# Kernel optimization log

Measured on AMD Instinct MI355X. Metric: run time of the kernel, lower is better.

The kernel has to match this reference:

```python
import jax, jax.numpy as jnp
import numpy as np

N_NODES = 50000
N_EDGES = 800000
IN_C = 16
HID_C = 16
OUT_C = 10
N_GRAPHS = 500
EDGE_DIM = 3
MLP_HID = 25
BN_EPS = 1e-5


def setup_inputs() -> dict:
    key = jax.random.key(0)
    ks = iter(jax.random.split(key, 40))

    def nrm(shape, scale=1.0):
        return jax.random.normal(next(ks), shape, dtype=jnp.float32) * scale

    inp = {}
    inp["x"] = nrm((N_NODES, IN_C))
    inp["edge_index"] = jax.random.randint(next(ks), (2, N_EDGES), 0, N_NODES, dtype=jnp.int32)
    inp["edge_attr"] = jax.random.uniform(next(ks), (N_EDGES, EDGE_DIM), dtype=jnp.float32)
    inp["batch"] = jnp.sort(jax.random.randint(next(ks), (N_NODES,), 0, N_GRAPHS, dtype=jnp.int32))

    def bn_params():
        g = jax.random.uniform(next(ks), (MLP_HID,), minval=0.8, maxval=1.2, dtype=jnp.float32)
        b = nrm((MLP_HID,), 0.1)
        mu = nrm((MLP_HID,), 0.1)
        var = jax.random.uniform(next(ks), (MLP_HID,), minval=0.5, maxval=1.5, dtype=jnp.float32)
        return g, b, mu, var

    # edge MLP 1: 3 -> 25 -> IN_C*HID_C
    inp["W1a"] = nrm((EDGE_DIM, MLP_HID), 0.3)
    inp["b1a"] = nrm((MLP_HID,), 0.05)
    inp["g1"], inp["bt1"], inp["m1"], inp["v1"] = bn_params()
    inp["W1b"] = nrm((MLP_HID, IN_C * HID_C), 0.1)
    inp["b1b"] = nrm((IN_C * HID_C,), 0.05)
    inp["root1"] = nrm((IN_C, HID_C), 0.2)
    inp["bias1"] = nrm((HID_C,), 0.05)

    # edge MLP 2: 3 -> 25 -> HID_C*HID_C
    inp["W2a"] = nrm((EDGE_DIM, MLP_HID), 0.3)
    inp["b2a"] = nrm((MLP_HID,), 0.05)
    inp["g2"], inp["bt2"], inp["m2"], inp["v2"] = bn_params()
    inp["W2b"] = nrm((MLP_HID, HID_C * HID_C), 0.1)
    inp["b2b"] = nrm((HID_C * HID_C,), 0.05)
    inp["root2"] = nrm((HID_C, HID_C), 0.2)
    inp["bias2"] = nrm((HID_C,), 0.05)

    # final MLP([HID_C, OUT_C]) -> single plain linear (plain_last)
    inp["fcW"] = nrm((HID_C, OUT_C), 0.2)
    inp["fcb"] = nrm((OUT_C,), 0.05)
    return inp


def _edge_mlp(e, Wa, ba, g, bt, mu, var, Wb, bb):
    # Linear -> BatchNorm(eval) -> ReLU -> (dropout=eval identity) -> Linear
    h = e @ Wa + ba
    h = g * (h - mu) * jax.lax.rsqrt(var + BN_EPS) + bt
    h = jax.nn.relu(h)
    return h @ Wb + bb


def _nnconv(x, src, dst, w_edge, root, bias, out_dim):
    # message: x_j [E,in] times per-edge weight [E,in,out]
    msg = jnp.einsum("ei,eio->eo", x[src], w_edge)
    agg = jax.ops.segment_sum(msg, dst, num_segments=N_NODES)
    deg = jax.ops.segment_sum(jnp.ones((src.shape[0],), msg.dtype), dst, num_segments=N_NODES)
    agg = agg / jnp.maximum(deg, 1.0)[:, None]  # mean aggregation
    return agg + x @ root + bias


def reference(x, edge_index, edge_attr, batch,
              W1a, b1a, g1, bt1, m1, v1, W1b, b1b, root1, bias1,
              W2a, b2a, g2, bt2, m2, v2, W2b, b2b, root2, bias2,
              fcW, fcb):
    src, dst = edge_index[0], edge_index[1]

    w1 = _edge_mlp(edge_attr, W1a, b1a, g1, bt1, m1, v1, W1b, b1b).reshape(-1, IN_C, HID_C)
    x = jax.nn.elu(_nnconv(x, src, dst, w1, root1, bias1, HID_C))

    w2 = _edge_mlp(edge_attr, W2a, b2a, g2, bt2, m2, v2, W2b, b2b).reshape(-1, HID_C, HID_C)
    x = jax.nn.elu(_nnconv(x, src, dst, w2, root2, bias2, HID_C))

    # global mean pooling over graphs
    pooled = jax.ops.segment_sum(x, batch, num_segments=N_GRAPHS)
    cnt = jax.ops.segment_sum(jnp.ones((x.shape[0],), x.dtype), batch, num_segments=N_GRAPHS)
    pooled = pooled / jnp.maximum(cnt, 1.0)[:, None]

    return pooled @ fcW + fcb  # [N_GRAPHS, OUT_C]
```

## Files before the change

kernel.cpp:

```cpp
#include <hip/hip_runtime.h>
#include <math.h>

#define N_NODES 50000
#define N_EDGES 800000
#define IN_C 16
#define HID_C 16
#define OUT_C 10
#define N_GRAPHS 500
#define EDGE_DIM 3
#define MLP_HID 25
#define BN_EPS 1e-5f

#define SCAN_NB ((N_NODES + 255) / 256)

typedef __attribute__((ext_vector_type(8))) _Float16 half8;
typedef __attribute__((ext_vector_type(2))) _Float16 half2v;
typedef __attribute__((ext_vector_type(4))) float f32x4;
union U4H8 { uint4 u; half8 h; half2v p[4]; };
union HU { _Float16 h; unsigned short u; };


__global__ __launch_bounds__(256) void setup_kernel(
    const float* __restrict__ W1a, const float* __restrict__ b1a,
    const float* __restrict__ g1, const float* __restrict__ bt1,
    const float* __restrict__ m1, const float* __restrict__ v1,
    const float* __restrict__ W2a, const float* __restrict__ b2a,
    const float* __restrict__ g2, const float* __restrict__ bt2,
    const float* __restrict__ m2, const float* __restrict__ v2,
    const float* __restrict__ W1b, const float* __restrict__ b1b,
    const float* __restrict__ W2b, const float* __restrict__ b2b,
    const int* __restrict__ batch,
    float* __restrict__ AC1, float* __restrict__ AC2,
    unsigned int* __restrict__ WF1, unsigned int* __restrict__ WF2,
    int* __restrict__ goff, int* __restrict__ cnt, int* __restrict__ ticket)
{
    const int blk = blockIdx.x;
    const int tid = threadIdx.x;
    if (blk < 7) {
        int t = blk * 256 + tid;
        if (t >= 1664) return;
        const float *Wb, *bb; unsigned int *WH;
        int tl = t;
        if (t < 832) { Wb = W1b; bb = b1b; WH = WF1; }
        else { tl = t - 832; Wb = W2b; bb = b2b; WH = WF2; }
        int m = tl >> 6;
        int L = tl & 63;
        int q = L >> 4, o = L & 15;
        unsigned int hi[8];
        for (int j = 0; j < 8; ++j) {
            int kp = m*32 + q*8 + j;
            int k = kp >> 4, i = kp & 15;
            float w = (k < 25) ? Wb[k*256 + i*16 + o] : bb[i*16 + o];
            HU cv; cv.h = (_Float16)w;
            hi[j] = cv.u;
        }
        int base = (m*64 + L) * 4;
        for (int d = 0; d < 4; ++d)
            WH[base + d] = hi[2*d] | (hi[2*d+1] << 16);
        return;
    }
    if (blk == 7 || blk == 8) {
        if (blk == 7) {
            if (tid < 26) {
                int k = tid;
                if (k < 25) {
                    float sc = g1[k] / sqrtf(v1[k] + BN_EPS);
                    AC1[k*4+0] = sc * W1a[0*MLP_HID+k];
                    AC1[k*4+1] = sc * W1a[1*MLP_HID+k];
                    AC1[k*4+2] = sc * W1a[2*MLP_HID+k];
                    AC1[k*4+3] = sc * (b1a[k] - m1[k]) + bt1[k];
                } else {
                    AC1[100] = 0.f; AC1[101] = 0.f; AC1[102] = 0.f; AC1[103] = 1.f;
                }
            } else if (tid >= 32 && tid < 58) {
                int k = tid - 32;
                if (k < 25) {
                    float sc = g2[k] / sqrtf(v2[k] + BN_EPS);
                    AC2[k*4+0] = sc * W2a[0*MLP_HID+k];
                    AC2[k*4+1] = sc * W2a[1*MLP_HID+k];
                    AC2[k*4+2] = sc * W2a[2*MLP_HID+k];
                    AC2[k*4+3] = sc * (b2a[k] - m2[k]) + bt2[k];
                } else {
                    AC2[100] = 0.f; AC2[101] = 0.f; AC2[102] = 0.f; AC2[103] = 1.f;
                }
            }
        }
        int g = (blk - 7) * 256 + tid;
        if (g <= N_GRAPHS) {
            int lo = 0, hi = N_NODES;
            while (lo < hi) {
                int mid = (lo + hi) >> 1;
                if (batch[mid] < g) lo = mid + 1; else hi = mid;
            }
            goff[g] = lo;
        }
        return;
    }
    int idx = (blk - 9) * 256 + tid;
    if (idx < N_NODES) cnt[idx] = 0;
    if (blk == 9 && tid == 0) *ticket = 0;
}


__global__ __launch_bounds__(256) void rank_kernel(const int* __restrict__ dst,
                                                   int* __restrict__ cnt,
                                                   int* __restrict__ rank) {
    int e = blockIdx.x * blockDim.x + threadIdx.x;
    if (e < N_EDGES) rank[e] = atomicAdd(&cnt[dst[e]], 1);
}

__global__ __launch_bounds__(256) void scan_p1(const int* __restrict__ cnt,
                                               int* __restrict__ bsum,
                                               int* __restrict__ bpre,
                                               int* __restrict__ off,
                                               int* __restrict__ ticket) {
    __shared__ int lds[256];
    __shared__ int sDone;
    int t = threadIdx.x;
    int idx = blockIdx.x * 256 + t;
    lds[t] = (idx < N_NODES) ? cnt[idx] : 0;
    __syncthreads();
    for (int d = 128; d > 0; d >>= 1) {
        if (t < d) lds[t] += lds[t + d];
        __syncthreads();
    }
    if (t == 0) {
        bsum[blockIdx.x] = lds[0];
        __threadfence();
        sDone = atomicAdd(ticket, 1);
    }
    __syncthreads();
    if (sDone != SCAN_NB - 1) return;
    __threadfence();
    int v = (t < SCAN_NB) ? bsum[t] : 0;
    __syncthreads();
    lds[t] = v;
    __syncthreads();
    for (int d = 1; d < 256; d <<= 1) {
        int u = (t >= d) ? lds[t - d] : 0;
        __syncthreads();
        lds[t] += u;
        __syncthreads();
    }
    if (t < SCAN_NB) bpre[t] = (t > 0) ? lds[t - 1] : 0;
    if (t == 255) off[N_NODES] = lds[255];
}

__global__ __launch_bounds__(256) void scan_p3(const int* __restrict__ cnt,
                                               const int* __restrict__ bpre,
                                               int* __restrict__ off) {
    __shared__ int lds[256];
    int t = threadIdx.x;
    int idx = blockIdx.x * 256 + t;
    int v = (idx < N_NODES) ? cnt[idx] : 0;
    lds[t] = v;
    __syncthreads();
    for (int d = 1; d < 256; d <<= 1) {
        int u = (t >= d) ? lds[t - d] : 0;
        __syncthreads();
        lds[t] += u;
        __syncthreads();
    }
    if (idx < N_NODES) off[idx] = bpre[blockIdx.x] + lds[t] - v;
}


__global__ __launch_bounds__(256) void edge_mfma6_kernel(
    const float* __restrict__ xin,
    const int* __restrict__ src,
    const int* __restrict__ dst,
    const int* __restrict__ rank,
    const int* __restrict__ off,
    const float* __restrict__ eattr,
    const float* __restrict__ AC,
    const unsigned int* __restrict__ WF,
    float* __restrict__ msg_buf)
{
    __shared__ uint4 wf_s[832];
    const int tid = threadIdx.x;
    #pragma unroll
    for (int it = 0; it < 4; ++it) {
        int gi = tid + it*256;
        if (gi < 832) wf_s[gi] = ((const uint4*)WF)[gi];
    }
    __syncthreads();

    const int wave = tid >> 6;
    const int lane = tid & 63;
    const int q    = lane >> 4;
    const int el   = lane & 15;
    const int i0   = (q & 1) * 8;
    const bool bsel = (q >> 1) != 0;
    const int E0   = (blockIdx.x * 4 + wave) * 64;

    const int sAll = src[E0 + lane];
    const int dAll = dst[E0 + lane];
    const int rAll = rank[E0 + lane];
    const int pAll = off[dAll] + rAll;

    int   sT[4];
    float a0[4], a1[4], a2[4];
    #pragma unroll
    for (int t = 0; t < 4; ++t) {
        sT[t] = __shfl(sAll, t*16 + el);
        int e = E0 + t*16 + el;
        a0[t] = eattr[(size_t)e*3+0];
        a1[t] = eattr[(size_t)e*3+1];
        a2[t] = eattr[(size_t)e*3+2];
    }

    U4H8 xf[4];
    #pragma unroll
    for (int t = 0; t < 4; ++t) {
        const float4* xp = (const float4*)(xin + (size_t)sT[t]*16 + i0);
        const float4 xl = xp[0], xh = xp[1];
        const float x8[8] = {xl.x,xl.y,xl.z,xl.w,xh.x,xh.y,xh.z,xh.w};
        #pragma unroll
        for (int j = 0; j < 4; ++j) {
            half2v tv; tv.x = (_Float16)x8[2*j]; tv.y = (_Float16)x8[2*j+1];
            xf[t].p[j] = tv;
        }
    }

    f32x4 acc0 = {0.f,0.f,0.f,0.f}, acc1 = {0.f,0.f,0.f,0.f};
    f32x4 acc2 = {0.f,0.f,0.f,0.f}, acc3 = {0.f,0.f,0.f,0.f};
    #pragma unroll 1
    for (int m = 0; m < 13; ++m) {
        const float4 Ae = *(const float4*)(AC + m*8);
        const float4 Ao = *(const float4*)(AC + m*8 + 4);
        const float A0 = bsel ? Ao.x : Ae.x;
        const float A1 = bsel ? Ao.y : Ae.y;
        const float A2 = bsel ? Ao.z : Ae.z;
        const float A3 = bsel ? Ao.w : Ae.w;
        U4H8 w; w.u = wf_s[m*64 + lane];
        #pragma unroll
        for (int t = 0; t < 4; ++t) {
            float h = fmaxf(fmaf(a2[t], A2, fmaf(a1[t], A1,
                              fmaf(a0[t], A0, A3))), 0.f);
            _Float16 hh = (_Float16)h;
            half2v h2; h2.x = hh; h2.y = hh;
            U4H8 f;
            #pragma unroll
            for (int j = 0; j < 4; ++j) f.p[j] = h2 * xf[t].p[j];
            f32x4 a = (t==0) ? acc0 : (t==1) ? acc1 : (t==2) ? acc2 : acc3;
            a = __builtin_amdgcn_mfma_f32_16x16x32_f16(w.h, f.h, a, 0, 0, 0);
            if (t==0) acc0 = a; else if (t==1) acc1 = a;
            else if (t==2) acc2 = a; else acc3 = a;
        }
    }

    #pragma unroll
    for (int t = 0; t < 4; ++t) {
        int row = __shfl(pAll, t*16 + el);
        f32x4 a = (t==0) ? acc0 : (t==1) ? acc1 : (t==2) ? acc2 : acc3;
        *(f32x4*)(msg_buf + (size_t)row * HID_C + q*4) = a;
    }
}

__global__ __launch_bounds__(256) void node_gather_kernel(
    const float* __restrict__ xin, const float* __restrict__ msg_buf,
    const int* __restrict__ off,
    const float* __restrict__ root, const float* __restrict__ bias,
    float* __restrict__ xout)
{
    int t = blockIdx.x * blockDim.x + threadIdx.x;
    int n = t >> 4;
    int o = t & 15;
    if (n >= N_NODES) return;
    int lo = off[n], hi = off[n+1];
    float inv = 1.f / fmaxf((float)(hi - lo), 1.f);

    float s0 = 0.f, s1 = 0.f, s2 = 0.f, s3 = 0.f;
    int r = lo;
    for (; r + 4 <= hi; r += 4) {
        s0 += msg_buf[(size_t)r     * HID_C + o];
        s1 += msg_buf[(size_t)(r+1) * HID_C + o];
        s2 += msg_buf[(size_t)(r+2) * HID_C + o];
        s3 += msg_buf[(size_t)(r+3) * HID_C + o];
    }
    for (; r < hi; ++r) s0 += msg_buf[(size_t)r * HID_C + o];
    float s = (s0 + s1) + (s2 + s3);

    float acc = fmaf(s, inv, bias[o]);
    const float* xr = xin + (size_t)n * IN_C;
    #pragma unroll
    for (int i = 0; i < IN_C; ++i)
        acc = fmaf(xr[i], root[i*HID_C+o], acc);
    xout[(size_t)n*HID_C + o] = acc > 0.f ? acc : (expf(acc) - 1.f);
}

__global__ __launch_bounds__(64) void pool_final_kernel(
    const float* __restrict__ xin, const int* __restrict__ goff,
    const float* __restrict__ fcW, const float* __restrict__ fcb,
    float* __restrict__ out)
{
    __shared__ float part[4][HID_C];
    __shared__ float pooled[HID_C];
    int g = blockIdx.x;
    int t = threadIdx.x;
    int c = t & 15, sub = t >> 4;
    int lo = goff[g], hi = goff[g+1];
    float s = 0.f;
    for (int n = lo + sub; n < hi; n += 4)
        s += xin[(size_t)n*HID_C + c];
    part[sub][c] = s;
    __syncthreads();
    if (t < HID_C) {
        pooled[t] = (part[0][t] + part[1][t] + part[2][t] + part[3][t])
                    / fmaxf((float)(hi - lo), 1.f);
    }
    __syncthreads();
    if (t < OUT_C) {
        float acc = fcb[t];
        #pragma unroll
        for (int i = 0; i < HID_C; ++i)
            acc = fmaf(pooled[i], fcW[i*OUT_C+t], acc);
        out[g*OUT_C + t] = acc;
    }
}


extern "C" void kernel_launch(void* const* d_in, const int* in_sizes, int n_in,
                              void* d_out, int out_size, void* d_ws, size_t ws_size,
                              hipStream_t stream)
{
    const float* x     = (const float*)d_in[0];
    const int*   ei    = (const int*)d_in[1];
    const float* eattr = (const float*)d_in[2];
    const int*   batch = (const int*)d_in[3];
    const float* W1a   = (const float*)d_in[4];
    const float* b1a   = (const float*)d_in[5];
    const float* g1    = (const float*)d_in[6];
    const float* bt1   = (const float*)d_in[7];
    const float* m1    = (const float*)d_in[8];
    const float* v1    = (const float*)d_in[9];
    const float* W1b   = (const float*)d_in[10];
    const float* b1b   = (const float*)d_in[11];
    const float* root1 = (const float*)d_in[12];
    const float* bias1 = (const float*)d_in[13];
    const float* W2a   = (const float*)d_in[14];
    const float* b2a   = (const float*)d_in[15];
    const float* g2    = (const float*)d_in[16];
    const float* bt2   = (const float*)d_in[17];
    const float* m2    = (const float*)d_in[18];
    const float* v2    = (const float*)d_in[19];
    const float* W2b   = (const float*)d_in[20];
    const float* b2b   = (const float*)d_in[21];
    const float* root2 = (const float*)d_in[22];
    const float* bias2 = (const float*)d_in[23];
    const float* fcW   = (const float*)d_in[24];
    const float* fcb   = (const float*)d_in[25];

    const int* src = ei;
    const int* dst = ei + N_EDGES;

    float* ws   = (float*)d_ws;
    float* MSG  = ws;
    float* X1   = ws + 12800000;
    float* X2   = ws + 13600000;
    int*   RANK = (int*)(ws + 14400000);
    int*   CNT  = (int*)(ws + 15200000);
    int*   OFF  = (int*)(ws + 15250000);
    int*   GOFF = (int*)(ws + 15300064);
    unsigned int* WF1 = (unsigned int*)(ws + 15300576);
    unsigned int* WF2 = (unsigned int*)(ws + 15303904);
    float* AC1  = ws + 15307232;
    float* AC2  = ws + 15307344;
    int*   BSUM = (int*)(ws + 15307456);
    int*   BPRE = (int*)(ws + 15307712);
    int*   TICK = (int*)(ws + 15307968);

    setup_kernel<<<9 + SCAN_NB, 256, 0, stream>>>(
        W1a, b1a, g1, bt1, m1, v1, W2a, b2a, g2, bt2, m2, v2,
        W1b, b1b, W2b, b2b, batch, AC1, AC2, WF1, WF2, GOFF, CNT, TICK);
    rank_kernel<<<N_EDGES/256, 256, 0, stream>>>(dst, CNT, RANK);
    scan_p1<<<SCAN_NB, 256, 0, stream>>>(CNT, BSUM, BPRE, OFF, TICK);
    scan_p3<<<SCAN_NB, 256, 0, stream>>>(CNT, BPRE, OFF);

    edge_mfma6_kernel<<<N_EDGES/256, 256, 0, stream>>>(x, src, dst, RANK, OFF,
                                                       eattr, AC1, WF1, MSG);
    node_gather_kernel<<<(N_NODES*16+255)/256, 256, 0, stream>>>(x, MSG, OFF,
                                                                 root1, bias1, X1);

    edge_mfma6_kernel<<<N_EDGES/256, 256, 0, stream>>>(X1, src, dst, RANK, OFF,
                                                       eattr, AC2, WF2, MSG);
    node_gather_kernel<<<(N_NODES*16+255)/256, 256, 0, stream>>>(X1, MSG, OFF,
                                                                 root2, bias2, X2);

    pool_final_kernel<<<N_GRAPHS, 64, 0, stream>>>(X2, GOFF, fcW, fcb, (float*)d_out);
}
```

Baseline: 260.5 us.

## Store edge messages in fp16 and fuse scan into single decoupled-lookback pass

Edge messages are now written as fp16 instead of fp32, halving the message buffer traffic for both the scatter write in the edge kernel and the gather reads in the node kernel. The two-kernel block scan is replaced by a single-pass scan using decoupled lookback with per-block flags, removing one launch and one reread of the counts. The fp16 messages lose precision before mean aggregation. The lookback spin relies on blocks being scheduled in order, which holds in practice but is not guaranteed.

```diff
diff --git a/kernel.cpp b/kernel.cpp
--- a/kernel.cpp
+++ b/kernel.cpp
@@ -18,6 +18,7 @@
 typedef __attribute__((ext_vector_type(4))) float f32x4;
 union U4H8 { uint4 u; half8 h; half2v p[4]; };
 union HU { _Float16 h; unsigned short u; };
+union H2U2 { half2v p[2]; uint2 u; };
 
 
 __global__ __launch_bounds__(256) void setup_kernel(
@@ -32,7 +33,7 @@
     const int* __restrict__ batch,
     float* __restrict__ AC1, float* __restrict__ AC2,
     unsigned int* __restrict__ WF1, unsigned int* __restrict__ WF2,
-    int* __restrict__ goff, int* __restrict__ cnt, int* __restrict__ ticket)
+    int* __restrict__ goff, int* __restrict__ cnt, int* __restrict__ flag)
 {
     const int blk = blockIdx.x;
     const int tid = threadIdx.x;
@@ -98,7 +99,7 @@
     }
     int idx = (blk - 9) * 256 + tid;
     if (idx < N_NODES) cnt[idx] = 0;
-    if (blk == 9 && tid == 0) *ticket = 0;
+    if (blk == 9 && tid < SCAN_NB) flag[tid] = 0;
 }
 
 
@@ -109,31 +110,16 @@
     if (e < N_EDGES) rank[e] = atomicAdd(&cnt[dst[e]], 1);
 }
 
-__global__ __launch_bounds__(256) void scan_p1(const int* __restrict__ cnt,
-                                               int* __restrict__ bsum,
-                                               int* __restrict__ bpre,
-                                               int* __restrict__ off,
-                                               int* __restrict__ ticket) {
+__global__ __launch_bounds__(256) void scan_single(const int* __restrict__ cnt,
+                                                   int* __restrict__ off,
+                                                   int* __restrict__ agg,
+                                                   int* __restrict__ pre,
+                                                   int* __restrict__ flag) {
     __shared__ int lds[256];
-    __shared__ int sDone;
-    int t = threadIdx.x;
-    int idx = blockIdx.x * 256 + t;
-    lds[t] = (idx < N_NODES) ? cnt[idx] : 0;
-    __syncthreads();
-    for (int d = 128; d > 0; d >>= 1) {
-        if (t < d) lds[t] += lds[t + d];
-        __syncthreads();
-    }
-    if (t == 0) {
-        bsum[blockIdx.x] = lds[0];
-        __threadfence();
-        sDone = atomicAdd(ticket, 1);
-    }
-    __syncthreads();
-    if (sDone != SCAN_NB - 1) return;
-    __threadfence();
-    int v = (t < SCAN_NB) ? bsum[t] : 0;
-    __syncthreads();
+    __shared__ int sExc;
+    const int b = blockIdx.x, t = threadIdx.x;
+    const int idx = b * 256 + t;
+    const int v = (idx < N_NODES) ? cnt[idx] : 0;
     lds[t] = v;
     __syncthreads();
     for (int d = 1; d < 256; d <<= 1) {
@@ -142,26 +128,35 @@
         lds[t] += u;
         __syncthreads();
     }
-    if (t < SCAN_NB) bpre[t] = (t > 0) ? lds[t - 1] : 0;
-    if (t == 255) off[N_NODES] = lds[255];
-}
-
-__global__ __launch_bounds__(256) void scan_p3(const int* __restrict__ cnt,
-                                               const int* __restrict__ bpre,
-                                               int* __restrict__ off) {
-    __shared__ int lds[256];
-    int t = threadIdx.x;
-    int idx = blockIdx.x * 256 + t;
-    int v = (idx < N_NODES) ? cnt[idx] : 0;
-    lds[t] = v;
-    __syncthreads();
-    for (int d = 1; d < 256; d <<= 1) {
-        int u = (t >= d) ? lds[t - d] : 0;
-        __syncthreads();
-        lds[t] += u;
-        __syncthreads();
-    }
-    if (idx < N_NODES) off[idx] = bpre[blockIdx.x] + lds[t] - v;
+    const int total = lds[255];
+    if (t == 0) {
+        int exc = 0;
+        if (b == 0) {
+            atomicExch(&pre[0], total);
+            __threadfence();
+            atomicExch(&flag[0], 2);
+        } else {
+            atomicExch(&agg[b], total);
+            __threadfence();
+            atomicExch(&flag[b], 1);
+            int j = b - 1;
+            while (true) {
+                int f;
+                do { f = atomicAdd(&flag[j], 0); } while (f == 0);
+                if (f == 2) { exc += atomicAdd(&pre[j], 0); break; }
+                exc += atomicAdd(&agg[j], 0);
+                --j;
+            }
+            atomicExch(&pre[b], exc + total);
+            __threadfence();
+            atomicExch(&flag[b], 2);
+        }
+        sExc = exc;
+    }
+    __syncthreads();
+    const int exc = sExc;
+    if (idx < N_NODES) off[idx] = exc + lds[t] - v;
+    if (b == SCAN_NB - 1 && t == 255) off[N_NODES] = exc + total;
 }
 
 
@@ -174,7 +169,7 @@
     const float* __restrict__ eattr,
     const float* __restrict__ AC,
     const unsigned int* __restrict__ WF,
-    float* __restrict__ msg_buf)
+    _Float16* __restrict__ msg_buf)
 {
     __shared__ uint4 wf_s[832];
     const int tid = threadIdx.x;
@@ -253,12 +248,16 @@
     for (int t = 0; t < 4; ++t) {
         int row = __shfl(pAll, t*16 + el);
         f32x4 a = (t==0) ? acc0 : (t==1) ? acc1 : (t==2) ? acc2 : acc3;
-        *(f32x4*)(msg_buf + (size_t)row * HID_C + q*4) = a;
+        H2U2 cv;
+        half2v c01; c01.x = (_Float16)a[0]; c01.y = (_Float16)a[1];
+        half2v c23; c23.x = (_Float16)a[2]; c23.y = (_Float16)a[3];
+        cv.p[0] = c01; cv.p[1] = c23;
+        *(uint2*)(msg_buf + (size_t)row * HID_C + q*4) = cv.u;
     }
 }
 
 __global__ __launch_bounds__(256) void node_gather_kernel(
-    const float* __restrict__ xin, const float* __restrict__ msg_buf,
+    const float* __restrict__ xin, const _Float16* __restrict__ msg_buf,
     const int* __restrict__ off,
     const float* __restrict__ root, const float* __restrict__ bias,
     float* __restrict__ xout)
@@ -273,12 +272,12 @@
     float s0 = 0.f, s1 = 0.f, s2 = 0.f, s3 = 0.f;
     int r = lo;
     for (; r + 4 <= hi; r += 4) {
-        s0 += msg_buf[(size_t)r     * HID_C + o];
-        s1 += msg_buf[(size_t)(r+1) * HID_C + o];
-        s2 += msg_buf[(size_t)(r+2) * HID_C + o];
-        s3 += msg_buf[(size_t)(r+3) * HID_C + o];
-    }
-    for (; r < hi; ++r) s0 += msg_buf[(size_t)r * HID_C + o];
+        s0 += (float)msg_buf[(size_t)r     * HID_C + o];
+        s1 += (float)msg_buf[(size_t)(r+1) * HID_C + o];
+        s2 += (float)msg_buf[(size_t)(r+2) * HID_C + o];
+        s3 += (float)msg_buf[(size_t)(r+3) * HID_C + o];
+    }
+    for (; r < hi; ++r) s0 += (float)msg_buf[(size_t)r * HID_C + o];
     float s = (s0 + s1) + (s2 + s3);
 
     float acc = fmaf(s, inv, bias[o]);
@@ -355,7 +354,7 @@
     const int* dst = ei + N_EDGES;
 
     float* ws   = (float*)d_ws;
-    float* MSG  = ws;
+    _Float16* MSG = (_Float16*)ws;
     float* X1   = ws + 12800000;
     float* X2   = ws + 13600000;
     int*   RANK = (int*)(ws + 14400000);
@@ -366,16 +365,15 @@
     unsigned int* WF2 = (unsigned int*)(ws + 15303904);
     float* AC1  = ws + 15307232;
     float* AC2  = ws + 15307344;
-    int*   BSUM = (int*)(ws + 15307456);
-    int*   BPRE = (int*)(ws + 15307712);
-    int*   TICK = (int*)(ws + 15307968);
+    int*   AGG  = (int*)(ws + 15307456);
+    int*   PRE  = (int*)(ws + 15307712);
+    int*   FLAG = (int*)(ws + 15307968);
 
     setup_kernel<<<9 + SCAN_NB, 256, 0, stream>>>(
         W1a, b1a, g1, bt1, m1, v1, W2a, b2a, g2, bt2, m2, v2,
-        W1b, b1b, W2b, b2b, batch, AC1, AC2, WF1, WF2, GOFF, CNT, TICK);
+        W1b, b1b, W2b, b2b, batch, AC1, AC2, WF1, WF2, GOFF, CNT, FLAG);
     rank_kernel<<<N_EDGES/256, 256, 0, stream>>>(dst, CNT, RANK);
-    scan_p1<<<SCAN_NB, 256, 0, stream>>>(CNT, BSUM, BPRE, OFF, TICK);
-    scan_p3<<<SCAN_NB, 256, 0, stream>>>(CNT, BPRE, OFF);
+    scan_single<<<SCAN_NB, 256, 0, stream>>>(CNT, OFF, AGG, PRE, FLAG);
 
     edge_mfma6_kernel<<<N_EDGES/256, 256, 0, stream>>>(x, src, dst, RANK, OFF,
                                                        eattr, AC1, WF1, MSG);
```

New measurement: 263.7 us. No clear change (+1.3%).
